# Kernel optimization log

Hardware: AMD Instinct MI355X
Metric: run time of the kernel (lower is better)

The kernel has to match this reference:

```python
import jax, jax.numpy as jnp
import numpy as np

N, E, F, H, C = 50000, 800000, 128, 256, 40
BN_EPS = 1e-5


def setup_inputs() -> dict:
    key = jax.random.key(0)
    ks = jax.random.split(key, 8)
    s = 0.05
    return {
        'x': jax.random.normal(ks[0], (N, F), jnp.float32),
        'edge_index': jax.random.randint(ks[1], (2, E), 0, N),
        'eps1': jnp.zeros((), jnp.float32),
        'W1': jax.random.normal(ks[2], (F, H), jnp.float32) * s,
        'b1': jnp.zeros((H,), jnp.float32),
        'g1': jnp.ones((H,), jnp.float32),
        'be1': jnp.zeros((H,), jnp.float32),
        'W2': jax.random.normal(ks[3], (H, H), jnp.float32) * s,
        'b2': jnp.zeros((H,), jnp.float32),
        'eps2': jnp.zeros((), jnp.float32),
        'W3': jax.random.normal(ks[4], (H, H), jnp.float32) * s,
        'b3': jnp.zeros((H,), jnp.float32),
        'g2': jnp.ones((H,), jnp.float32),
        'be2': jnp.zeros((H,), jnp.float32),
        'W4': jax.random.normal(ks[5], (H, H), jnp.float32) * s,
        'b4': jnp.zeros((H,), jnp.float32),
        'g3': jnp.ones((H,), jnp.float32),
        'be3': jnp.zeros((H,), jnp.float32),
        'Wf': jax.random.normal(ks[6], (H, C), jnp.float32) * s,
        'bf': jnp.zeros((C,), jnp.float32),
    }


def _bn(h, g, b):
    # BatchNorm1d forward with batch statistics (training-mode math, biased var)
    m = jnp.mean(h, axis=0)
    v = jnp.var(h, axis=0)
    return (h - m) * jax.lax.rsqrt(v + BN_EPS) * g + b


def _gin_conv(x, edge_index, eps, Wa, ba, g, be, Wb, bb):
    # GINConv: out = mlp((1+eps)*x + sum_{(src->dst)} x[src])
    src, dst = edge_index[0], edge_index[1]
    agg = jax.ops.segment_sum(x[src], dst, num_segments=x.shape[0])  # [N, d]
    h = (1.0 + eps) * x + agg
    h = jnp.maximum(_bn(h @ Wa + ba, g, be), 0.0)  # Linear-BN-ReLU
    return h @ Wb + bb                              # Linear


def reference(x, edge_index, eps1, W1, b1, g1, be1, W2, b2,
              eps2, W3, b3, g2, be2, W4, b4, g3, be3, Wf, bf):
    h = _gin_conv(x, edge_index, eps1, W1, b1, g1, be1, W2, b2)
    h = jnp.maximum(h, 0.0)  # F.relu (dropout p=0)
    h = _gin_conv(h, edge_index, eps2, W3, b3, g2, be2, W4, b4)
    h = jnp.maximum(_bn(h, g3, be3), 0.0)  # bn2 + relu
    return h @ Wf + bf  # fc -> [N, C]
```

## Files before the change

### kernel.cpp

```cpp
#include <hip/hip_runtime.h>
#include <hip/hip_bf16.h>


#define NN 50000
#define EE 800000
#define FDIM 128
#define HDIM 256
#define CDIM 40
#define BN_EPS 1e-5f

typedef unsigned short u16;
typedef unsigned int u32;
typedef __attribute__((ext_vector_type(8))) short short8;
typedef __attribute__((ext_vector_type(4))) float f32x4;

__device__ __forceinline__ float bflo(u32 u) { return __uint_as_float(u << 16); }
__device__ __forceinline__ float bfhi(u32 u) { return __uint_as_float(u & 0xFFFF0000u); }
__device__ __forceinline__ u16 f2bf(float f) {
  __hip_bfloat16 h = __float2bfloat16(f);
  return *(u16*)&h;
}
__device__ __forceinline__ u32 pack2(float a, float b) {
  return (u32)f2bf(a) | ((u32)f2bf(b) << 16);
}

__global__ void k_hist(const int* __restrict__ ei, int* __restrict__ deg) {
  int e = blockIdx.x * 256 + threadIdx.x;
  if (e < EE) atomicAdd(&deg[ei[EE + e]], 1);
}

__global__ void k_scan_blocks(const int* __restrict__ in, int* __restrict__ partial,
                              int* __restrict__ bsums, int n) {
  __shared__ int s[256];
  int i = blockIdx.x * 256 + threadIdx.x;
  s[threadIdx.x] = (i < n) ? in[i] : 0;
  __syncthreads();
  for (int d = 1; d < 256; d <<= 1) {
    int t = (threadIdx.x >= d) ? s[threadIdx.x - d] : 0;
    __syncthreads();
    s[threadIdx.x] += t;
    __syncthreads();
  }
  if (i < n) partial[i] = s[threadIdx.x];
  if (threadIdx.x == 255) bsums[blockIdx.x] = s[255];
}

__global__ void k_scan_sums(int* __restrict__ bs, int nb) {
  __shared__ int s[256];
  s[threadIdx.x] = (threadIdx.x < nb) ? bs[threadIdx.x] : 0;
  __syncthreads();
  for (int d = 1; d < 256; d <<= 1) {
    int t = (threadIdx.x >= d) ? s[threadIdx.x - d] : 0;
    __syncthreads();
    s[threadIdx.x] += t;
    __syncthreads();
  }
  int ex = (threadIdx.x == 0) ? 0 : s[threadIdx.x - 1];
  if (threadIdx.x < nb) bs[threadIdx.x] = ex;
}

__global__ void k_scan_add(const int* __restrict__ partial, const int* __restrict__ bs,
                           const int* __restrict__ deg,
                           int* __restrict__ rowstart, int* __restrict__ cursor, int n) {
  int i = blockIdx.x * 256 + threadIdx.x;
  if (i < n) {
    int incl = partial[i] + bs[blockIdx.x];
    rowstart[i + 1] = incl;
    cursor[i] = incl - deg[i];
  }
  if (i == 0) rowstart[0] = 0;
}

__global__ void k_scatter(const int* __restrict__ ei, int* __restrict__ cursor,
                          int* __restrict__ sorted_src) {
  int e = blockIdx.x * 256 + threadIdx.x;
  if (e < EE) {
    int dst = ei[EE + e];
    int p = atomicAdd(&cursor[dst], 1);
    sorted_src[p] = ei[e];
  }
}

__global__ void k_cvt_x(const float* __restrict__ x, u16* __restrict__ xb,
                        int* __restrict__ deg, float* __restrict__ stats) {
  int i = blockIdx.x * 256 + threadIdx.x;
  if (i < NN) deg[i] = 0;
  if (i < 6 * 256) stats[i] = 0.f;
  size_t base = (size_t)i * 4;
  if (base < (size_t)NN * FDIM) {
    float4 v = *(const float4*)&x[base];
    *(uint2*)&xb[base] = make_uint2(pack2(v.x, v.y), pack2(v.z, v.w));
  }
}

__global__ void k_cvt_w(const float* __restrict__ W1, const float* __restrict__ W2,
                        const float* __restrict__ W3, const float* __restrict__ W4,
                        const float* __restrict__ Wf,
                        u16* __restrict__ W1t, u16* __restrict__ W2t,
                        u16* __restrict__ W3t, u16* __restrict__ W4t,
                        u16* __restrict__ Wft) {
  int b = blockIdx.x, t = threadIdx.x;
  if (b < 128) {
    int i = b * 256 + t; int k = i >> 8, n = i & 255;
    W1t[(size_t)n * 128 + (((k >> 3) ^ (n & 7)) << 3) + (k & 7)] = f2bf(W1[i]);
  } else if (b < 384) {
    int i = (b - 128) * 256 + t; int k = i >> 8, n = i & 255;
    W2t[(size_t)n * 256 + (((k >> 3) ^ (n & 7)) << 3) + (k & 7)] = f2bf(W2[i]);
  } else if (b < 640) {
    int i = (b - 384) * 256 + t; int k = i >> 8, n = i & 255;
    W3t[(size_t)n * 256 + (((k >> 3) ^ (n & 7)) << 3) + (k & 7)] = f2bf(W3[i]);
  } else if (b < 896) {
    int i = (b - 640) * 256 + t; int k = i >> 8, n = i & 255;
    W4t[(size_t)n * 256 + (((k >> 3) ^ (n & 7)) << 3) + (k & 7)] = f2bf(W4[i]);
  } else {
    int j = (b - 896) * 256 + t;
    int c = j >> 8, k = j & 255;
    float v = (c < CDIM) ? Wf[(size_t)k * CDIM + c] : 0.f;
    Wft[(size_t)c * 256 + (((k >> 3) ^ (c & 7)) << 3) + (k & 7)] = f2bf(v);
  }
}

template <int FEAT>
__global__ __launch_bounds__(256)
void k_agg(const u16* __restrict__ x, const int* __restrict__ rowstart,
           const int* __restrict__ sorted_src, const float* __restrict__ epsp,
           u16* __restrict__ out) {
  int node = blockIdx.x * 4 + (threadIdx.x >> 6);
  if (node >= NN) return;
  int lane = threadIdx.x & 63;
  float e1 = 1.0f + epsp[0];
  int s = rowstart[node], t = rowstart[node + 1];
  if constexpr (FEAT == 128) {
    const u32* xp = (const u32*)x;
    u32 u = xp[(size_t)node * 64 + lane];
    float a0 = bflo(u) * e1, a1 = bfhi(u) * e1;
    int p = s;
    for (; p + 7 < t; p += 8) {
      u32 uu[8];
#pragma unroll
      for (int i = 0; i < 8; ++i) uu[i] = xp[(size_t)sorted_src[p + i] * 64 + lane];
#pragma unroll
      for (int i = 0; i < 8; ++i) { a0 += bflo(uu[i]); a1 += bfhi(uu[i]); }
    }
    for (; p < t; ++p) {
      u32 u0 = xp[(size_t)sorted_src[p] * 64 + lane];
      a0 += bflo(u0); a1 += bfhi(u0);
    }
    ((u32*)out)[(size_t)node * 64 + lane] = pack2(a0, a1);
  } else {
    const uint2* xp = (const uint2*)x;
    uint2 u = xp[(size_t)node * 64 + lane];
    float a0 = bflo(u.x) * e1, a1 = bfhi(u.x) * e1;
    float a2 = bflo(u.y) * e1, a3 = bfhi(u.y) * e1;
    int p = s;
    for (; p + 7 < t; p += 8) {
      uint2 uu[8];
#pragma unroll
      for (int i = 0; i < 8; ++i) uu[i] = xp[(size_t)sorted_src[p + i] * 64 + lane];
#pragma unroll
      for (int i = 0; i < 8; ++i) {
        a0 += bflo(uu[i].x); a1 += bfhi(uu[i].x);
        a2 += bflo(uu[i].y); a3 += bfhi(uu[i].y);
      }
    }
    for (; p < t; ++p) {
      uint2 u0 = xp[(size_t)sorted_src[p] * 64 + lane];
      a0 += bflo(u0.x); a1 += bfhi(u0.x);
      a2 += bflo(u0.y); a3 += bfhi(u0.y);
    }
    ((uint2*)out)[(size_t)node * 64 + lane] = make_uint2(pack2(a0, a1), pack2(a2, a3));
  }
}

template <int K, bool TRANSFORM, bool RELU_OUT, bool COLSUMS>
__global__ __launch_bounds__(512, 4)
void k_gemm(const u16* __restrict__ A, const u16* __restrict__ Wt,
            const float* __restrict__ bias,
            const float* __restrict__ icsum, const float* __restrict__ icsq,
            const float* __restrict__ g, const float* __restrict__ be,
            u16* __restrict__ C, float* __restrict__ ocsum, float* __restrict__ ocsq) {
  __shared__ u16 SMEM[128 * 64 + 256 * 64];
  __shared__ float2 Tb[TRANSFORM ? 256 : 1];
  u16* Asm = SMEM;
  u16* Bsm = SMEM + 128 * 64;

  const int tid = threadIdx.x;
  const int lane = tid & 63;
  const int w = tid >> 6;
  const int wm = w >> 2, wn = w & 3;
  const int lr = lane & 15, lq = lane >> 4;
  const int r0 = blockIdx.x * 128;

  if constexpr (TRANSFORM) {
    if (tid < 256) {
      float m = icsum[tid] * (1.0f / NN);
      float var = icsq[tid] * (1.0f / NN) - m * m;
      float s = g[tid] * rsqrtf(var + BN_EPS);
      Tb[tid] = make_float2(s, be[tid] - m * s);
    }
    __syncthreads();
  }

  f32x4 acc[4][4];
#pragma unroll
  for (int mi = 0; mi < 4; ++mi)
#pragma unroll
    for (int ni = 0; ni < 4; ++ni) acc[mi][ni] = (f32x4){0.f, 0.f, 0.f, 0.f};

  const int srow = tid >> 3;
  const int sc = tid & 7;

  for (int k0 = 0; k0 < K; k0 += 64) {
    if (k0 > 0) __syncthreads();
#pragma unroll
    for (int it = 0; it < 2; ++it) {
      int row = it * 64 + srow;
      int gr = r0 + row;
      int grc = gr < NN ? gr : NN - 1;
      short8 va = *(const short8*)&A[(size_t)grc * K + k0 + sc * 8];
      if constexpr (TRANSFORM) {
#pragma unroll
        for (int j = 0; j < 8; ++j) {
          float2 tb = Tb[k0 + sc * 8 + j];
          float f = fmaxf(fmaf(__uint_as_float(((u32)(u16)va[j]) << 16), tb.x, tb.y), 0.f);
          va[j] = (short)f2bf(f);
        }
      }
      ((short8*)Asm)[row * 8 + (sc ^ (row & 7))] = va;
    }
#pragma unroll
    for (int it = 0; it < 4; ++it) {
      int row = it * 64 + srow;
      short8 vb = *(const short8*)&Wt[(size_t)row * K + k0 + sc * 8];
      ((short8*)Bsm)[row * 8 + sc] = vb;
    }
    __syncthreads();

#pragma unroll
    for (int ks = 0; ks < 2; ++ks) {
      short8 af[4], bfx[4];
#pragma unroll
      for (int mi = 0; mi < 4; ++mi) {
        int row = wm * 64 + mi * 16 + lr;
        af[mi] = ((const short8*)Asm)[row * 8 + ((ks * 4 + lq) ^ (row & 7))];
      }
#pragma unroll
      for (int ni = 0; ni < 4; ++ni) {
        int rn = wn * 64 + ni * 16 + lr;
        bfx[ni] = ((const short8*)Bsm)[rn * 8 + ((ks * 4 + lq) ^ (rn & 7))];
      }
#pragma unroll
      for (int mi = 0; mi < 4; ++mi)
#pragma unroll
        for (int ni = 0; ni < 4; ++ni)
          acc[mi][ni] = __builtin_amdgcn_mfma_f32_16x16x32_bf16(af[mi], bfx[ni], acc[mi][ni], 0, 0, 0);
    }
  }
  __syncthreads();

  float bv[4];
#pragma unroll
  for (int ni = 0; ni < 4; ++ni) bv[ni] = bias[wn * 64 + ni * 16 + lr];
  float colS[4] = {}, colQ[4] = {};

  u16* Cs = SMEM;
#pragma unroll
  for (int r = 0; r < 2; ++r) {
    if (wm == r) {
#pragma unroll
      for (int mi = 0; mi < 4; ++mi)
#pragma unroll
        for (int ni = 0; ni < 4; ++ni) {
          int col = wn * 64 + ni * 16 + lr;
#pragma unroll
          for (int j = 0; j < 4; ++j) {
            int lrow = mi * 16 + lq * 4 + j;
            float v = acc[mi][ni][j] + bv[ni];
            if constexpr (RELU_OUT) v = fmaxf(v, 0.f);
            if constexpr (COLSUMS) {
              if (r0 + r * 64 + lrow < NN) { colS[ni] += v; colQ[ni] += v * v; }
            }
            Cs[lrow * 256 + col] = f2bf(v);
          }
        }
    }
    __syncthreads();
    {
      int lrow = tid >> 3;
      int gr = r0 + r * 64 + lrow;
      if (gr < NN) {
        int co = (tid & 7) * 32;
#pragma unroll
        for (int i = 0; i < 4; ++i)
          *(uint4*)&C[(size_t)gr * 256 + co + i * 8] = *(const uint4*)&Cs[lrow * 256 + co + i * 8];
      }
    }
    __syncthreads();
  }

  if constexpr (COLSUMS) {
#pragma unroll
    for (int ni = 0; ni < 4; ++ni) {
      float s = colS[ni], q = colQ[ni];
      s += __shfl_xor(s, 16); s += __shfl_xor(s, 32);
      q += __shfl_xor(q, 16); q += __shfl_xor(q, 32);
      if (lq == 0) {
        int col = wn * 64 + ni * 16 + lr;
        atomicAdd(&ocsum[col], s);
        atomicAdd(&ocsq[col], q);
      }
    }
  }
}

__global__ __launch_bounds__(512)
void k_final(const u16* __restrict__ z3, const u16* __restrict__ Wft,
             const float* __restrict__ bfp,
             const float* __restrict__ icsum, const float* __restrict__ icsq,
             const float* __restrict__ g, const float* __restrict__ be,
             float* __restrict__ out) {
  __shared__ u16 Bs[48 * 256];
  __shared__ float2 Tb[256];
  const int tid = threadIdx.x;
  const int lane = tid & 63;
  const int w = tid >> 6;
  const int lr = lane & 15, lq = lane >> 4;
  const int r0 = blockIdx.x * 128;

  int row = r0 + w * 16 + lr;
  int rc = row < NN ? row : NN - 1;
  const u16* Ap = &z3[(size_t)rc * 256];
  short8 a[8];
#pragma unroll
  for (int ks = 0; ks < 8; ++ks)
    a[ks] = *(const short8*)&Ap[(ks * 4 + lq) * 8];

  {
    const short8* Bv = (const short8*)Wft;
    short8* Bl = (short8*)Bs;
#pragma unroll
    for (int i = 0; i < 3; ++i)
      Bl[tid + i * 512] = Bv[tid + i * 512];
  }
  if (tid < 256) {
    float m = icsum[tid] * (1.0f / NN);
    float var = icsq[tid] * (1.0f / NN) - m * m;
    float s = g[tid] * rsqrtf(var + BN_EPS);
    Tb[tid] = make_float2(s, be[tid] - m * s);
  }
  __syncthreads();

  f32x4 acc[3];
#pragma unroll
  for (int ni = 0; ni < 3; ++ni) acc[ni] = (f32x4){0.f, 0.f, 0.f, 0.f};
#pragma unroll
  for (int ks = 0; ks < 8; ++ks) {
    short8 t0 = a[ks];
    int kb = (ks * 4 + lq) * 8;
#pragma unroll
    for (int j = 0; j < 8; ++j) {
      float2 tb = Tb[kb + j];
      float f0 = fmaxf(fmaf(__uint_as_float(((u32)(u16)t0[j]) << 16), tb.x, tb.y), 0.f);
      t0[j] = (short)f2bf(f0);
    }
#pragma unroll
    for (int ni = 0; ni < 3; ++ni) {
      int col = ni * 16 + lr;
      short8 bfr = *(const short8*)&Bs[(size_t)col * 256 + (((ks * 4 + lq) ^ (col & 7)) << 3)];
      acc[ni] = __builtin_amdgcn_mfma_f32_16x16x32_bf16(t0, bfr, acc[ni], 0, 0, 0);
    }
  }

#pragma unroll
  for (int ni = 0; ni < 3; ++ni) {
    int col = ni * 16 + lr;
    if (col < CDIM) {
      float bfv = bfp[col];
#pragma unroll
      for (int j = 0; j < 4; ++j) {
        int gr = r0 + w * 16 + lq * 4 + j;
        if (gr < NN) out[(size_t)gr * CDIM + col] = acc[ni][j] + bfv;
      }
    }
  }
}

extern "C" void kernel_launch(void* const* d_in, const int* in_sizes, int n_in,
                              void* d_out, int out_size, void* d_ws, size_t ws_size,
                              hipStream_t stream) {
  const float* x   = (const float*)d_in[0];
  const int*   ei  = (const int*)d_in[1];
  const float* eps1= (const float*)d_in[2];
  const float* W1  = (const float*)d_in[3];
  const float* b1  = (const float*)d_in[4];
  const float* g1  = (const float*)d_in[5];
  const float* be1 = (const float*)d_in[6];
  const float* W2  = (const float*)d_in[7];
  const float* b2  = (const float*)d_in[8];
  const float* eps2= (const float*)d_in[9];
  const float* W3  = (const float*)d_in[10];
  const float* b3  = (const float*)d_in[11];
  const float* g2  = (const float*)d_in[12];
  const float* be2 = (const float*)d_in[13];
  const float* W4  = (const float*)d_in[14];
  const float* b4  = (const float*)d_in[15];
  const float* g3  = (const float*)d_in[16];
  const float* be3 = (const float*)d_in[17];
  const float* Wf  = (const float*)d_in[18];
  const float* bf  = (const float*)d_in[19];
  float* out = (float*)d_out;

  char* p = (char*)d_ws;
  auto alloc = [&](size_t bytes) -> char* {
    char* r = p;
    p += (bytes + 255) & ~(size_t)255;
    return r;
  };
  float* stats   = (float*)alloc(6 * 256 * sizeof(float));
  int* deg       = (int*)alloc(NN * sizeof(int));
  int* rowstart  = (int*)alloc((NN + 16) * sizeof(int));
  int* cursor    = (int*)alloc(NN * sizeof(int));
  int* sorted    = (int*)alloc(EE * sizeof(int));
  int* partial   = (int*)alloc(NN * sizeof(int));
  int* bsums     = (int*)alloc(1024 * sizeof(int));
  u16* W1t       = (u16*)alloc(256 * 128 * sizeof(u16));
  u16* W2t       = (u16*)alloc(256 * 256 * sizeof(u16));
  u16* W3t       = (u16*)alloc(256 * 256 * sizeof(u16));
  u16* W4t       = (u16*)alloc(256 * 256 * sizeof(u16));
  u16* Wft       = (u16*)alloc(48 * 256 * sizeof(u16));
  u16* xb        = (u16*)alloc((size_t)NN * 128 * sizeof(u16));
  u16* A1        = (u16*)alloc((size_t)NN * 128 * sizeof(u16));
  u16* z1        = (u16*)alloc((size_t)NN * 256 * sizeof(u16));
  u16* h1        = (u16*)alloc((size_t)NN * 256 * sizeof(u16));
  u16* A2        = (u16*)alloc((size_t)NN * 256 * sizeof(u16));
  (void)alloc(64 * 1024);
  u16* z2 = z1;
  u16* z3 = h1;

  float* s1 = stats + 0,    *q1 = stats + 256;
  float* s2 = stats + 512,  *q2 = stats + 768;
  float* s3 = stats + 1024, *q3 = stats + 1280;

  const int nbE = (EE + 255) / 256;
  const int nbN = (NN + 255) / 256;

  k_cvt_x<<<(NN * FDIM / 4 + 255) / 256, 256, 0, stream>>>(x, xb, deg, stats);
  k_cvt_w<<<944, 256, 0, stream>>>(W1, W2, W3, W4, Wf, W1t, W2t, W3t, W4t, Wft);
  k_hist<<<nbE, 256, 0, stream>>>(ei, deg);
  k_scan_blocks<<<nbN, 256, 0, stream>>>(deg, partial, bsums, NN);
  k_scan_sums<<<1, 256, 0, stream>>>(bsums, nbN);
  k_scan_add<<<nbN, 256, 0, stream>>>(partial, bsums, deg, rowstart, cursor, NN);
  k_scatter<<<nbE, 256, 0, stream>>>(ei, cursor, sorted);

  const int gGemm = (NN + 127) / 128;

  k_agg<128><<<(NN + 3) / 4, 256, 0, stream>>>(xb, rowstart, sorted, eps1, A1);
  k_gemm<128, false, false, true><<<gGemm, 512, 0, stream>>>(
      A1, W1t, b1, nullptr, nullptr, nullptr, nullptr, z1, s1, q1);
  k_gemm<256, true, true, false><<<gGemm, 512, 0, stream>>>(
      z1, W2t, b2, s1, q1, g1, be1, h1, nullptr, nullptr);

  k_agg<256><<<(NN + 3) / 4, 256, 0, stream>>>(h1, rowstart, sorted, eps2, A2);
  k_gemm<256, false, false, true><<<gGemm, 512, 0, stream>>>(
      A2, W3t, b3, nullptr, nullptr, nullptr, nullptr, z2, s2, q2);
  k_gemm<256, true, false, true><<<gGemm, 512, 0, stream>>>(
      z2, W4t, b4, s2, q2, g2, be2, z3, s3, q3);

  k_final<<<(NN + 127) / 128, 512, 0, stream>>>(z3, Wft, bf, s3, q3, g3, be3, out);
}
```

Baseline: 336.3 us.

## Split GEMM over N halves, use global_load_lds, fuse preprocessing kernels

After: 357.0 us. +6.1%, slower.

```diff
diff --git a/kernel.cpp b/kernel.cpp
--- a/kernel.cpp
+++ b/kernel.cpp
@@ -24,9 +24,10 @@
   return (u32)f2bf(a) | ((u32)f2bf(b) << 16);
 }
 
-__global__ void k_hist(const int* __restrict__ ei, int* __restrict__ deg) {
-  int e = blockIdx.x * 256 + threadIdx.x;
-  if (e < EE) atomicAdd(&deg[ei[EE + e]], 1);
+__device__ __forceinline__ void gld16(const u16* g, u16* l) {
+  __builtin_amdgcn_global_load_lds(
+      (const __attribute__((address_space(1))) void*)g,
+      (__attribute__((address_space(3))) void*)l, 16, 0, 0);
 }
 
 __global__ void k_scan_blocks(const int* __restrict__ in, int* __restrict__ partial,
@@ -81,42 +82,45 @@
   }
 }
 
-__global__ void k_cvt_x(const float* __restrict__ x, u16* __restrict__ xb,
-                        int* __restrict__ deg, float* __restrict__ stats) {
-  int i = blockIdx.x * 256 + threadIdx.x;
-  if (i < NN) deg[i] = 0;
-  if (i < 6 * 256) stats[i] = 0.f;
-  size_t base = (size_t)i * 4;
-  if (base < (size_t)NN * FDIM) {
+#define NB_CVTX 6250
+#define NB_CVTW 944
+#define NB_HIST 3125
+__global__ void k_pre(const float* __restrict__ x, u16* __restrict__ xb,
+                      const int* __restrict__ ei, int* __restrict__ deg,
+                      const float* __restrict__ W1, const float* __restrict__ W2,
+                      const float* __restrict__ W3, const float* __restrict__ W4,
+                      const float* __restrict__ Wf,
+                      u16* __restrict__ W1t, u16* __restrict__ W2t,
+                      u16* __restrict__ W3t, u16* __restrict__ W4t,
+                      u16* __restrict__ Wft) {
+  int b = blockIdx.x, t = threadIdx.x;
+  if (b < NB_CVTX) {
+    size_t base = ((size_t)b * 256 + t) * 4;
     float4 v = *(const float4*)&x[base];
     *(uint2*)&xb[base] = make_uint2(pack2(v.x, v.y), pack2(v.z, v.w));
-  }
-}
-
-__global__ void k_cvt_w(const float* __restrict__ W1, const float* __restrict__ W2,
-                        const float* __restrict__ W3, const float* __restrict__ W4,
-                        const float* __restrict__ Wf,
-                        u16* __restrict__ W1t, u16* __restrict__ W2t,
-                        u16* __restrict__ W3t, u16* __restrict__ W4t,
-                        u16* __restrict__ Wft) {
-  int b = blockIdx.x, t = threadIdx.x;
-  if (b < 128) {
-    int i = b * 256 + t; int k = i >> 8, n = i & 255;
-    W1t[(size_t)n * 128 + (((k >> 3) ^ (n & 7)) << 3) + (k & 7)] = f2bf(W1[i]);
-  } else if (b < 384) {
-    int i = (b - 128) * 256 + t; int k = i >> 8, n = i & 255;
-    W2t[(size_t)n * 256 + (((k >> 3) ^ (n & 7)) << 3) + (k & 7)] = f2bf(W2[i]);
-  } else if (b < 640) {
-    int i = (b - 384) * 256 + t; int k = i >> 8, n = i & 255;
-    W3t[(size_t)n * 256 + (((k >> 3) ^ (n & 7)) << 3) + (k & 7)] = f2bf(W3[i]);
-  } else if (b < 896) {
-    int i = (b - 640) * 256 + t; int k = i >> 8, n = i & 255;
-    W4t[(size_t)n * 256 + (((k >> 3) ^ (n & 7)) << 3) + (k & 7)] = f2bf(W4[i]);
+  } else if (b < NB_CVTX + NB_CVTW) {
+    int bb = b - NB_CVTX;
+    if (bb < 128) {
+      int i = bb * 256 + t; int k = i >> 8, n = i & 255;
+      W1t[(size_t)n * 128 + (((k >> 3) ^ (n & 7)) << 3) + (k & 7)] = f2bf(W1[i]);
+    } else if (bb < 384) {
+      int i = (bb - 128) * 256 + t; int k = i >> 8, n = i & 255;
+      W2t[(size_t)n * 256 + (((k >> 3) ^ (n & 7)) << 3) + (k & 7)] = f2bf(W2[i]);
+    } else if (bb < 640) {
+      int i = (bb - 384) * 256 + t; int k = i >> 8, n = i & 255;
+      W3t[(size_t)n * 256 + (((k >> 3) ^ (n & 7)) << 3) + (k & 7)] = f2bf(W3[i]);
+    } else if (bb < 896) {
+      int i = (bb - 640) * 256 + t; int k = i >> 8, n = i & 255;
+      W4t[(size_t)n * 256 + (((k >> 3) ^ (n & 7)) << 3) + (k & 7)] = f2bf(W4[i]);
+    } else {
+      int j = (bb - 896) * 256 + t;
+      int c = j >> 8, k = j & 255;
+      float v = (c < CDIM) ? Wf[(size_t)k * CDIM + c] : 0.f;
+      Wft[(size_t)c * 256 + (((k >> 3) ^ (c & 7)) << 3) + (k & 7)] = f2bf(v);
+    }
   } else {
-    int j = (b - 896) * 256 + t;
-    int c = j >> 8, k = j & 255;
-    float v = (c < CDIM) ? Wf[(size_t)k * CDIM + c] : 0.f;
-    Wft[(size_t)c * 256 + (((k >> 3) ^ (c & 7)) << 3) + (k & 7)] = f2bf(v);
+    int e = (b - NB_CVTX - NB_CVTW) * 256 + t;
+    atomicAdd(&deg[ei[EE + e]], 1);
   }
 }
 
@@ -173,13 +177,13 @@
 }
 
 template <int K, bool TRANSFORM, bool RELU_OUT, bool COLSUMS>
-__global__ __launch_bounds__(512, 4)
+__global__ __launch_bounds__(256, 4)
 void k_gemm(const u16* __restrict__ A, const u16* __restrict__ Wt,
             const float* __restrict__ bias,
             const float* __restrict__ icsum, const float* __restrict__ icsq,
             const float* __restrict__ g, const float* __restrict__ be,
             u16* __restrict__ C, float* __restrict__ ocsum, float* __restrict__ ocsq) {
-  __shared__ u16 SMEM[128 * 64 + 256 * 64];
+  __shared__ u16 SMEM[128 * 128];
   __shared__ float2 Tb[TRANSFORM ? 256 : 1];
   u16* Asm = SMEM;
   u16* Bsm = SMEM + 128 * 64;
@@ -187,17 +191,16 @@
   const int tid = threadIdx.x;
   const int lane = tid & 63;
   const int w = tid >> 6;
-  const int wm = w >> 2, wn = w & 3;
+  const int wm = w >> 1, wn = w & 1;
   const int lr = lane & 15, lq = lane >> 4;
-  const int r0 = blockIdx.x * 128;
+  const int r0 = (blockIdx.x >> 1) * 128;
+  const int n0 = (blockIdx.x & 1) * 128;
 
   if constexpr (TRANSFORM) {
-    if (tid < 256) {
-      float m = icsum[tid] * (1.0f / NN);
-      float var = icsq[tid] * (1.0f / NN) - m * m;
-      float s = g[tid] * rsqrtf(var + BN_EPS);
-      Tb[tid] = make_float2(s, be[tid] - m * s);
-    }
+    float m = icsum[tid] * (1.0f / NN);
+    float var = icsq[tid] * (1.0f / NN) - m * m;
+    float s = g[tid] * rsqrtf(var + BN_EPS);
+    Tb[tid] = make_float2(s, be[tid] - m * s);
     __syncthreads();
   }
 
@@ -207,32 +210,39 @@
 #pragma unroll
     for (int ni = 0; ni < 4; ++ni) acc[mi][ni] = (f32x4){0.f, 0.f, 0.f, 0.f};
 
-  const int srow = tid >> 3;
-  const int sc = tid & 7;
-
   for (int k0 = 0; k0 < K; k0 += 64) {
-    if (k0 > 0) __syncthreads();
-#pragma unroll
-    for (int it = 0; it < 2; ++it) {
-      int row = it * 64 + srow;
-      int gr = r0 + row;
-      int grc = gr < NN ? gr : NN - 1;
-      short8 va = *(const short8*)&A[(size_t)grc * K + k0 + sc * 8];
-      if constexpr (TRANSFORM) {
+#pragma unroll
+    for (int i = 0; i < 4; ++i) {
+      int slot = i * 256 + tid;
+      int r = slot >> 3, c = slot & 7;
+      gld16(&Wt[(size_t)(n0 + r) * K + k0 + c * 8], &Bsm[(size_t)(i * 256 + (tid & ~63)) * 8]);
+    }
+    if constexpr (!TRANSFORM) {
+#pragma unroll
+      for (int i = 0; i < 4; ++i) {
+        int slot = i * 256 + tid;
+        int r = slot >> 3, c = slot & 7;
+        int gr = r0 + r;
+        int grc = gr < NN ? gr : NN - 1;
+        gld16(&A[(size_t)grc * K + k0 + ((c ^ (r & 7)) << 3)],
+              &Asm[(size_t)(i * 256 + (tid & ~63)) * 8]);
+      }
+    } else {
+#pragma unroll
+      for (int i = 0; i < 4; ++i) {
+        int slot = i * 256 + tid;
+        int r = slot >> 3, c = slot & 7;
+        int gr = r0 + r;
+        int grc = gr < NN ? gr : NN - 1;
+        short8 va = *(const short8*)&A[(size_t)grc * K + k0 + c * 8];
 #pragma unroll
         for (int j = 0; j < 8; ++j) {
-          float2 tb = Tb[k0 + sc * 8 + j];
+          float2 tb = Tb[k0 + c * 8 + j];
           float f = fmaxf(fmaf(__uint_as_float(((u32)(u16)va[j]) << 16), tb.x, tb.y), 0.f);
           va[j] = (short)f2bf(f);
         }
-      }
-      ((short8*)Asm)[row * 8 + (sc ^ (row & 7))] = va;
-    }
-#pragma unroll
-    for (int it = 0; it < 4; ++it) {
-      int row = it * 64 + srow;
-      short8 vb = *(const short8*)&Wt[(size_t)row * K + k0 + sc * 8];
-      ((short8*)Bsm)[row * 8 + sc] = vb;
+        ((short8*)Asm)[r * 8 + (c ^ (r & 7))] = va;
+      }
     }
     __syncthreads();
 
@@ -255,47 +265,42 @@
         for (int ni = 0; ni < 4; ++ni)
           acc[mi][ni] = __builtin_amdgcn_mfma_f32_16x16x32_bf16(af[mi], bfx[ni], acc[mi][ni], 0, 0, 0);
     }
-  }
+    __syncthreads();
+  }
+
+  float bv[4];
+#pragma unroll
+  for (int ni = 0; ni < 4; ++ni) bv[ni] = bias[n0 + wn * 64 + ni * 16 + lr];
+  float colS[4] = {}, colQ[4] = {};
+
+  u16* Cs = SMEM;
+#pragma unroll
+  for (int mi = 0; mi < 4; ++mi)
+#pragma unroll
+    for (int ni = 0; ni < 4; ++ni) {
+      int col = wn * 64 + ni * 16 + lr;
+#pragma unroll
+      for (int j = 0; j < 4; ++j) {
+        int row = wm * 64 + mi * 16 + lq * 4 + j;
+        float v = acc[mi][ni][j] + bv[ni];
+        if constexpr (RELU_OUT) v = fmaxf(v, 0.f);
+        if constexpr (COLSUMS) {
+          if (r0 + row < NN) { colS[ni] += v; colQ[ni] += v * v; }
+        }
+        Cs[row * 128 + col] = f2bf(v);
+      }
+    }
   __syncthreads();
 
-  float bv[4];
-#pragma unroll
-  for (int ni = 0; ni < 4; ++ni) bv[ni] = bias[wn * 64 + ni * 16 + lr];
-  float colS[4] = {}, colQ[4] = {};
-
-  u16* Cs = SMEM;
-#pragma unroll
-  for (int r = 0; r < 2; ++r) {
-    if (wm == r) {
-#pragma unroll
-      for (int mi = 0; mi < 4; ++mi)
-#pragma unroll
-        for (int ni = 0; ni < 4; ++ni) {
-          int col = wn * 64 + ni * 16 + lr;
-#pragma unroll
-          for (int j = 0; j < 4; ++j) {
-            int lrow = mi * 16 + lq * 4 + j;
-            float v = acc[mi][ni][j] + bv[ni];
-            if constexpr (RELU_OUT) v = fmaxf(v, 0.f);
-            if constexpr (COLSUMS) {
-              if (r0 + r * 64 + lrow < NN) { colS[ni] += v; colQ[ni] += v * v; }
-            }
-            Cs[lrow * 256 + col] = f2bf(v);
-          }
-        }
-    }
-    __syncthreads();
-    {
-      int lrow = tid >> 3;
-      int gr = r0 + r * 64 + lrow;
-      if (gr < NN) {
-        int co = (tid & 7) * 32;
-#pragma unroll
-        for (int i = 0; i < 4; ++i)
-          *(uint4*)&C[(size_t)gr * 256 + co + i * 8] = *(const uint4*)&Cs[lrow * 256 + co + i * 8];
-      }
-    }
-    __syncthreads();
+#pragma unroll
+  for (int p = 0; p < 4; ++p) {
+    int row = p * 32 + (tid >> 3);
+    int gr = r0 + row;
+    if (gr < NN) {
+      int co = (tid & 7) * 16;
+      *(uint4*)&C[(size_t)gr * 256 + n0 + co] = *(const uint4*)&Cs[row * 128 + co];
+      *(uint4*)&C[(size_t)gr * 256 + n0 + co + 8] = *(const uint4*)&Cs[row * 128 + co + 8];
+    }
   }
 
   if constexpr (COLSUMS) {
@@ -305,7 +310,7 @@
       s += __shfl_xor(s, 16); s += __shfl_xor(s, 32);
       q += __shfl_xor(q, 16); q += __shfl_xor(q, 32);
       if (lq == 0) {
-        int col = wn * 64 + ni * 16 + lr;
+        int col = n0 + wn * 64 + ni * 16 + lr;
         atomicAdd(&ocsum[col], s);
         atomicAdd(&ocsq[col], q);
       }
@@ -441,29 +446,29 @@
   float* s2 = stats + 512,  *q2 = stats + 768;
   float* s3 = stats + 1024, *q3 = stats + 1280;
 
-  const int nbE = (EE + 255) / 256;
   const int nbN = (NN + 255) / 256;
 
-  k_cvt_x<<<(NN * FDIM / 4 + 255) / 256, 256, 0, stream>>>(x, xb, deg, stats);
-  k_cvt_w<<<944, 256, 0, stream>>>(W1, W2, W3, W4, Wf, W1t, W2t, W3t, W4t, Wft);
-  k_hist<<<nbE, 256, 0, stream>>>(ei, deg);
+  hipMemsetAsync(stats, 0, 6 * 256 * sizeof(float) + NN * sizeof(int), stream);
+
+  k_pre<<<NB_CVTX + NB_CVTW + NB_HIST, 256, 0, stream>>>(
+      x, xb, ei, deg, W1, W2, W3, W4, Wf, W1t, W2t, W3t, W4t, Wft);
   k_scan_blocks<<<nbN, 256, 0, stream>>>(deg, partial, bsums, NN);
   k_scan_sums<<<1, 256, 0, stream>>>(bsums, nbN);
   k_scan_add<<<nbN, 256, 0, stream>>>(partial, bsums, deg, rowstart, cursor, NN);
-  k_scatter<<<nbE, 256, 0, stream>>>(ei, cursor, sorted);
-
-  const int gGemm = (NN + 127) / 128;
+  k_scatter<<<(EE + 255) / 256, 256, 0, stream>>>(ei, cursor, sorted);
+
+  const int gGemm = ((NN + 127) / 128) * 2;
 
   k_agg<128><<<(NN + 3) / 4, 256, 0, stream>>>(xb, rowstart, sorted, eps1, A1);
-  k_gemm<128, false, false, true><<<gGemm, 512, 0, stream>>>(
+  k_gemm<128, false, false, true><<<gGemm, 256, 0, stream>>>(
       A1, W1t, b1, nullptr, nullptr, nullptr, nullptr, z1, s1, q1);
-  k_gemm<256, true, true, false><<<gGemm, 512, 0, stream>>>(
+  k_gemm<256, true, true, false><<<gGemm, 256, 0, stream>>>(
       z1, W2t, b2, s1, q1, g1, be1, h1, nullptr, nullptr);
 
   k_agg<256><<<(NN + 3) / 4, 256, 0, stream>>>(h1, rowstart, sorted, eps2, A2);
-  k_gemm<256, false, false, true><<<gGemm, 512, 0, stream>>>(
+  k_gemm<256, false, false, true><<<gGemm, 256, 0, stream>>>(
       A2, W3t, b3, nullptr, nullptr, nullptr, nullptr, z2, s2, q2);
-  k_gemm<256, true, false, true><<<gGemm, 512, 0, stream>>>(
+  k_gemm<256, true, false, true><<<gGemm, 256, 0, stream>>>(
       z2, W4t, b4, s2, q2, g2, be2, z3, s3, q3);
 
   k_final<<<(NN + 127) / 128, 512, 0, stream>>>(z3, Wft, bf, s3, q3, g3, be3, out);
```
